# Optimization experiments

Measured on AMD Instinct MI355X. Metric: run time of the kernel, lower is better.

## Reference

```python
import jax, jax.numpy as jnp
import numpy as np
import math

B, S, E, H, D, L, HF = 8, 1024, 512, 8, 64, 6, 2048
EPS = 1e-5
INF = 1000000.0


def _gelu(x):
    # custom tanh-approx gelu from the source
    return 0.5 * x * (1 + jnp.tanh(math.sqrt(2 / math.pi) * (x + 0.044715 * x ** 3)))


def _layernorm(x, gamma, beta):
    mean = jnp.mean(x, axis=-1, keepdims=True)
    var = jnp.mean((x - mean) ** 2, axis=-1, keepdims=True)
    return gamma * ((x - mean) / jnp.sqrt(var + EPS)) + beta


def setup_inputs() -> dict:
    key = jax.random.key(0)
    ks = jax.random.split(key, 10)
    scale = 0.02
    x = jax.random.normal(ks[0], (B, S, E), dtype=jnp.float32)
    att_mask = jax.random.randint(ks[1], (B, S), 0, 2) == 1
    WQ = jax.random.normal(ks[2], (L, E, E), dtype=jnp.float32) * scale
    WK = jax.random.normal(ks[3], (L, E, E), dtype=jnp.float32) * scale
    WV = jax.random.normal(ks[4], (L, E, E), dtype=jnp.float32) * scale
    WO = jax.random.normal(ks[5], (L, E, E), dtype=jnp.float32) * scale
    W1 = jax.random.normal(ks[6], (L, HF, E), dtype=jnp.float32) * scale
    W2 = jax.random.normal(ks[7], (L, E, HF), dtype=jnp.float32) * scale
    bQ = jnp.zeros((L, E)); bK = jnp.zeros((L, E)); bV = jnp.zeros((L, E)); bO = jnp.zeros((L, E))
    b1 = jnp.zeros((L, HF)); b2 = jnp.zeros((L, E))
    g1 = jnp.ones((L, E)); bt1 = jnp.zeros((L, E))
    g2 = jnp.ones((L, E)); bt2 = jnp.zeros((L, E))
    return {"x": x, "att_mask": att_mask, "WQ": WQ, "bQ": bQ, "WK": WK, "bK": bK,
            "WV": WV, "bV": bV, "WO": WO, "bO": bO, "W1": W1, "b1": b1, "W2": W2,
            "b2": b2, "g1": g1, "bt1": bt1, "g2": g2, "bt2": bt2}


def reference(x, att_mask, WQ, bQ, WK, bK, WV, bV, WO, bO, W1, b1, W2, b2, g1, bt1, g2, bt2):
    # additive mask applied to scores: score - (~mask) * infinity, broadcast over (B,1,1,S)
    inv_att = (~att_mask).astype(x.dtype)[:, None, None, :] * INF
    inv_sqrt_d = 1.0 / math.sqrt(D)
    for l in range(L):
        # --- multi-head self-attention ---
        q = (jnp.einsum('bse,fe->bsf', x, WQ[l]) + bQ[l]).reshape(B, S, H, D).transpose(0, 2, 1, 3)
        k = (jnp.einsum('bse,fe->bsf', x, WK[l]) + bK[l]).reshape(B, S, H, D).transpose(0, 2, 1, 3)
        v = (jnp.einsum('bse,fe->bsf', x, WV[l]) + bV[l]).reshape(B, S, H, D).transpose(0, 2, 1, 3)
        score = jnp.einsum('bhsd,bhtd->bhst', q, k) * inv_sqrt_d - inv_att
        attn = jax.nn.softmax(score, axis=-1)
        o = jnp.einsum('bhst,bhtd->bhsd', attn, v).transpose(0, 2, 1, 3).reshape(B, S, E)
        o = jnp.einsum('bse,fe->bsf', o, WO[l]) + bO[l]
        x = _layernorm(x + o, g1[l], bt1[l])
        # --- pointwise feed-forward ---
        h = _gelu(jnp.einsum('bse,fe->bsf', x, W1[l]) + b1[l])
        f = jnp.einsum('bsf,ef->bse', h, W2[l]) + b2[l]
        x = _layernorm(x + f, g2[l], bt2[l])
    return x
```

## Files before the change

kernel.cpp:

```cpp
#include <hip/hip_runtime.h>
#include <cstdint>
#include <cstddef>

#define NB 8
#define NS 1024
#define NE 512
#define NH 8
#define ND 64
#define NL 6
#define NHF 2048
#define NROW (NB*NS)

typedef __bf16 bf16_t;
typedef __bf16 bf8v __attribute__((ext_vector_type(8)));
typedef __bf16 bf4v __attribute__((ext_vector_type(4)));
typedef float  f4   __attribute__((ext_vector_type(4)));

extern "C" __device__ float __ocml_native_exp2_f32(float);
#define EXP2F __ocml_native_exp2_f32
#define LOG2E 1.4426950408889634f

__device__ __forceinline__ void async_copy16(const bf16_t* g, bf16_t* l) {
    __builtin_amdgcn_global_load_lds(
        (const __attribute__((address_space(1))) void*)g,
        (__attribute__((address_space(3))) void*)l,
        16, 0, 0);
}

__device__ __forceinline__ float gelu_f(float x) {
    const float s = fmaf(0.044715f * x * x, x, x);
    const float e = EXP2F(-2.3022081995f * s);
    return x * __builtin_amdgcn_rcpf(1.0f + e);
}

template<int BN, int ACT, int OUT>
__device__ __forceinline__ void gemm_core(
    bf16_t* __restrict__ sm,
    const bf16_t* __restrict__ A, const bf16_t* __restrict__ Bm,
    const float* __restrict__ bias, bf16_t* __restrict__ Cb,
    int m0, int n0, int N, int K)
{
    constexpr int JN = BN / 32, WSPAN = BN / 2;
    bf16_t* As = sm;
    bf16_t* Bs = sm + 2*128*64;
    const int tid  = threadIdx.x;
    const int lane = tid & 63;
    const int wave = tid >> 6;
    const int wm = wave >> 1, wn = wave & 1;
    const int quad = lane >> 4, l16 = lane & 15;
    const int srow = tid >> 3;
    const int scol = (((tid & 7) ^ (srow & 7)) << 3);

    f4 acc[4][JN] = {};

    const bf16_t* Ag = A  + (size_t)(m0 + srow) * K + scol;
    const bf16_t* Bg = Bm + (size_t)(n0 + srow) * K + scol;
    const int sw = (l16 & 7);

    auto stage = [&](int buf, int kt) {
#pragma unroll
        for (int r = 0; r < 4; ++r)
            async_copy16(Ag + (size_t)r * 32 * K + kt, As + buf*8192 + tid*8 + r*2048);
#pragma unroll
        for (int r = 0; r < BN/32; ++r)
            async_copy16(Bg + (size_t)r * 32 * K + kt, Bs + buf*(BN*64) + tid*8 + r*2048);
    };

    stage(0, 0);
    int buf = 0;
    for (int kt = 0; kt < K; kt += 64, buf ^= 1) {
        __syncthreads();
        if (kt + 64 < K) stage(buf ^ 1, kt + 64);
        const bf16_t* Ab = As + buf*8192;
        const bf16_t* Bb = Bs + buf*(BN*64);
#pragma unroll
        for (int s = 0; s < 2; ++s) {
            const int c8 = ((s*4 + quad) ^ sw) * 8;
            bf8v af[4], bfv[JN];
#pragma unroll
            for (int i = 0; i < 4; ++i)
                af[i] = *(const bf8v*)(Ab + (wm*64 + i*16 + l16)*64 + c8);
#pragma unroll
            for (int j = 0; j < JN; ++j)
                bfv[j] = *(const bf8v*)(Bb + (wn*WSPAN + j*16 + l16)*64 + c8);
#pragma unroll
            for (int i = 0; i < 4; ++i)
#pragma unroll
                for (int j = 0; j < JN; ++j)
                    acc[i][j] = __builtin_amdgcn_mfma_f32_16x16x32_bf16(bfv[j], af[i], acc[i][j], 0, 0, 0);
        }
    }

#pragma unroll
    for (int i = 0; i < 4; ++i) {
        const int mi = m0 + wm*64 + i*16 + l16;
        const size_t m = (size_t)mi;
#pragma unroll
        for (int j = 0; j < JN; ++j) {
            const int nb = n0 + wn*WSPAN + j*16 + quad*4;
            const f4 bv = *(const f4*)(bias + nb);
            f4 v = acc[i][j] + bv;
            if (ACT) {
#pragma unroll
                for (int r = 0; r < 4; ++r) v[r] = gelu_f(v[r]);
            }
            bf4v* cp = (bf4v*)(Cb + m * (size_t)N + nb);
            bf4v o;
            if (OUT == 2) {
                const bf4v old = *cp;
#pragma unroll
                for (int r = 0; r < 4; ++r) o[r] = (bf16_t)((float)old[r] + v[r]);
            } else {
#pragma unroll
                for (int r = 0; r < 4; ++r) o[r] = (bf16_t)v[r];
            }
            *cp = o;
        }
    }
}

template<int BN, int ACT, int OUT>
__global__ __launch_bounds__(256)
void gemm_bt_k(const bf16_t* __restrict__ A, const bf16_t* __restrict__ Bm,
               const float* __restrict__ bias, bf16_t* __restrict__ Cb, int N, int K)
{
    __shared__ __align__(16) bf16_t smem[2*128*64 + 2*BN*64];
    gemm_core<BN, ACT, OUT>(smem, A, Bm, bias, Cb,
                            blockIdx.x * 128, blockIdx.y * BN, N, K);
}

__global__ __launch_bounds__(256, 2)
void gemm_qkv_k(const bf16_t* __restrict__ A,
                const bf16_t* __restrict__ wq, const bf16_t* __restrict__ wk, const bf16_t* __restrict__ wv,
                const float* __restrict__ bq, const float* __restrict__ bk, const float* __restrict__ bv,
                bf16_t* __restrict__ Q, bf16_t* __restrict__ K, bf16_t* __restrict__ Vt,
                const unsigned short* __restrict__ rank)
{
    __shared__ __align__(16) bf16_t As_[2*128*64];
    __shared__ __align__(16) bf16_t Bs_[3][2*64*64];
    const int tid  = threadIdx.x;
    const int lane = tid & 63;
    const int wave = tid >> 6;
    const int wm = wave >> 1, wn = wave & 1;
    const int quad = lane >> 4, l16 = lane & 15;
    const int sw = l16 & 7;
    const int srow = tid >> 3;
    const int scol = (((tid & 7) ^ (srow & 7)) << 3);
    const int m0 = blockIdx.x * 128, n0 = blockIdx.y * 64;

    const bf16_t* Ag = A + (size_t)(m0 + srow) * NE + scol;
    const bf16_t* Wg0 = wq + (size_t)(n0 + srow) * NE + scol;
    const bf16_t* Wg1 = wk + (size_t)(n0 + srow) * NE + scol;
    const bf16_t* Wg2 = wv + (size_t)(n0 + srow) * NE + scol;

    f4 acc[3][4][2] = {};

    auto stage = [&](int buf, int kt) {
#pragma unroll
        for (int r = 0; r < 4; ++r)
            async_copy16(Ag + (size_t)r*32*NE + kt, As_ + buf*8192 + tid*8 + r*2048);
#pragma unroll
        for (int r = 0; r < 2; ++r) {
            async_copy16(Wg0 + (size_t)r*32*NE + kt, Bs_[0] + buf*4096 + tid*8 + r*2048);
            async_copy16(Wg1 + (size_t)r*32*NE + kt, Bs_[1] + buf*4096 + tid*8 + r*2048);
            async_copy16(Wg2 + (size_t)r*32*NE + kt, Bs_[2] + buf*4096 + tid*8 + r*2048);
        }
    };

    stage(0, 0);
    int buf = 0;
    for (int kt = 0; kt < NE; kt += 64, buf ^= 1) {
        __syncthreads();
        if (kt + 64 < NE) stage(buf ^ 1, kt + 64);
        const bf16_t* Ab = As_ + buf*8192;
#pragma unroll
        for (int s = 0; s < 2; ++s) {
            const int c8 = ((s*4 + quad) ^ sw) * 8;
            bf8v af[4];
#pragma unroll
            for (int i = 0; i < 4; ++i)
                af[i] = *(const bf8v*)(Ab + (wm*64 + i*16 + l16)*64 + c8);
#pragma unroll
            for (int mat = 0; mat < 3; ++mat) {
                const bf16_t* Bb = Bs_[mat] + buf*4096;
                const bf8v b0 = *(const bf8v*)(Bb + (wn*32      + l16)*64 + c8);
                const bf8v b1 = *(const bf8v*)(Bb + (wn*32 + 16 + l16)*64 + c8);
                if (mat < 2) {
#pragma unroll
                    for (int i = 0; i < 4; ++i) {
                        acc[mat][i][0] = __builtin_amdgcn_mfma_f32_16x16x32_bf16(b0, af[i], acc[mat][i][0], 0, 0, 0);
                        acc[mat][i][1] = __builtin_amdgcn_mfma_f32_16x16x32_bf16(b1, af[i], acc[mat][i][1], 0, 0, 0);
                    }
                } else {
#pragma unroll
                    for (int i = 0; i < 4; ++i) {
                        acc[2][i][0] = __builtin_amdgcn_mfma_f32_16x16x32_bf16(af[i], b0, acc[2][i][0], 0, 0, 0);
                        acc[2][i][1] = __builtin_amdgcn_mfma_f32_16x16x32_bf16(af[i], b1, acc[2][i][1], 0, 0, 0);
                    }
                }
            }
        }
    }

#pragma unroll
    for (int i = 0; i < 4; ++i) {
        const int mi = m0 + wm*64 + i*16 + l16;
        const int mk = (mi & ~1023) + (int)rank[mi];
#pragma unroll
        for (int j = 0; j < 2; ++j) {
            const int nb = n0 + wn*32 + j*16 + quad*4;
            const f4 vq = acc[0][i][j] + *(const f4*)(bq + nb);
            const f4 vk = acc[1][i][j] + *(const f4*)(bk + nb);
            bf4v oq, ok;
#pragma unroll
            for (int r = 0; r < 4; ++r) { oq[r] = (bf16_t)vq[r]; ok[r] = (bf16_t)vk[r]; }
            *(bf4v*)(Q + (size_t)mi * NE + nb) = oq;
            *(bf4v*)(K + (size_t)mk * NE + nb) = ok;
        }
    }
#pragma unroll
    for (int j = 0; j < 2; ++j) {
        const int n = n0 + wn*32 + j*16 + l16;
        const float bvv = bv[n];
#pragma unroll
        for (int i = 0; i < 4; ++i) {
            const int mbase = m0 + wm*64 + i*16 + quad*4;
            const size_t b8h = (size_t)((mbase >> 10)*8 + (n >> 6));
            bf16_t* rowp = Vt + (b8h*64 + (size_t)(n & 63))*1024;
#pragma unroll
            for (int r = 0; r < 4; ++r)
                rowp[rank[mbase + r]] = (bf16_t)(acc[2][i][j][r] + bvv);
        }
    }
}

template<int ACT, int OUT>
__device__ __forceinline__ void gemm256_core(
    bf16_t* __restrict__ sm,
    const bf16_t* __restrict__ A, const bf16_t* __restrict__ Bm,
    const float* __restrict__ bias, bf16_t* __restrict__ Cb,
    int m0, int n0, int N, int K)
{
    const int tid  = threadIdx.x;
    const int lane = tid & 63;
    const int wave = tid >> 6;
    const int wm = wave >> 2, wn = wave & 3;
    const int quad = lane >> 4, l16 = lane & 15;
    const int sw = l16 & 7;
    const int srow = tid >> 3;
    const int scol = ((tid & 7) ^ (srow & 7)) << 3;

    bf16_t* As = sm;
    bf16_t* Bs = sm + 4 * 8192;

    const bf16_t* Ag = A  + (size_t)(m0 + srow) * K + scol;
    const bf16_t* Bg = Bm + (size_t)(n0 + srow) * K + scol;

    auto stageA = [&](int d, int h, int kt) {
        bf16_t* dst = As + (d*2 + h) * 8192 + tid * 8;
        const bf16_t* src = Ag + (size_t)(h * 128) * K + kt;
        async_copy16(src, dst);
        async_copy16(src + (size_t)64 * K, dst + 4096);
    };
    auto stageB = [&](int d, int h, int kt) {
        bf16_t* dst = Bs + (d*2 + h) * 8192 + tid * 8;
        const bf16_t* src = Bg + (size_t)(h * 128) * K + kt;
        async_copy16(src, dst);
        async_copy16(src + (size_t)64 * K, dst + 4096);
    };

    const int nt = K >> 6;

    f4 acc[8][4] = {};
    bf8v bfr[4][2], al[4][2], ah[4][2];

    auto mfmaQ = [&](const bf8v (&af)[4][2], int fb, int gb) {
#pragma unroll
        for (int kh = 0; kh < 2; ++kh)
#pragma unroll
            for (int f = 0; f < 4; ++f)
#pragma unroll
                for (int g = 0; g < 2; ++g)
                    acc[fb+f][gb+g] = __builtin_amdgcn_mfma_f32_16x16x32_bf16(bfr[gb+g][kh], af[f][kh], acc[fb+f][gb+g], 0, 0, 0);
    };

    stageB(0, 0, 0);  stageB(0, 1, 0);  stageA(0, 0, 0);  stageA(0, 1, 0);
    stageB(1, 0, 64); stageB(1, 1, 64); stageA(1, 0, 64);
    asm volatile("s_waitcnt vmcnt(6)" ::: "memory");
    __builtin_amdgcn_s_barrier();

    for (int t = 0; t < nt; ++t) {
        const int d = t & 1;
        const int kt2 = (t + 2) << 6;
        const bf16_t* Ab = As + (d*2 + wm) * 8192;
        const bf16_t* Bb = Bs + (d*2 + (wn >> 1)) * 8192 + (wn & 1) * 4096;

#pragma unroll
        for (int g = 0; g < 4; ++g)
#pragma unroll
            for (int kh = 0; kh < 2; ++kh)
                bfr[g][kh] = *(const bf8v*)(Bb + (g*16 + l16)*64 + (((kh*4 + quad) ^ sw) << 3));
#pragma unroll
        for (int f = 0; f < 4; ++f)
#pragma unroll
            for (int kh = 0; kh < 2; ++kh)
                al[f][kh] = *(const bf8v*)(Ab + (f*16 + l16)*64 + (((kh*4 + quad) ^ sw) << 3));
        if (t + 1 < nt) stageA(d ^ 1, 1, (t + 1) << 6);
        __builtin_amdgcn_s_barrier();
        __builtin_amdgcn_s_setprio(1);
        mfmaQ(al, 0, 0);
        __builtin_amdgcn_s_setprio(0);
        asm volatile("s_waitcnt lgkmcnt(0)" ::: "memory");
        __builtin_amdgcn_s_barrier();

#pragma unroll
        for (int f = 0; f < 4; ++f)
#pragma unroll
            for (int kh = 0; kh < 2; ++kh)
                ah[f][kh] = *(const bf8v*)(Ab + ((f + 4)*16 + l16)*64 + (((kh*4 + quad) ^ sw) << 3));
        if (t + 2 < nt) stageB(d, 0, kt2);
        __builtin_amdgcn_s_barrier();
        __builtin_amdgcn_s_setprio(1);
        mfmaQ(ah, 4, 0);
        __builtin_amdgcn_s_setprio(0);
        asm volatile("s_waitcnt lgkmcnt(0)" ::: "memory");
        __builtin_amdgcn_s_barrier();

        if (t + 2 < nt) stageB(d, 1, kt2);
        __builtin_amdgcn_s_barrier();
        __builtin_amdgcn_s_setprio(1);
        mfmaQ(al, 0, 2);
        __builtin_amdgcn_s_setprio(0);
        asm volatile("s_waitcnt lgkmcnt(0)" ::: "memory");
        __builtin_amdgcn_s_barrier();

        if (t + 2 < nt) stageA(d, 0, kt2);
        __builtin_amdgcn_s_barrier();
        __builtin_amdgcn_s_setprio(1);
        mfmaQ(ah, 4, 2);
        __builtin_amdgcn_s_setprio(0);
        asm volatile("s_waitcnt lgkmcnt(0)" ::: "memory");
        if (t + 1 < nt) {
            if (t + 2 < nt) asm volatile("s_waitcnt vmcnt(6)" ::: "memory");
            else            asm volatile("s_waitcnt vmcnt(0)" ::: "memory");
        }
        __builtin_amdgcn_s_barrier();
    }

#pragma unroll
    for (int f = 0; f < 8; ++f) {
        const int mi = m0 + wm*128 + f*16 + l16;
        const size_t m = (size_t)mi;
#pragma unroll
        for (int g = 0; g < 4; ++g) {
            const int nb = n0 + wn*64 + g*16 + quad*4;
            const f4 bv = *(const f4*)(bias + nb);
            f4 v = acc[f][g] + bv;
            if (ACT) {
#pragma unroll
                for (int r = 0; r < 4; ++r) v[r] = gelu_f(v[r]);
            }
            bf4v* cp = (bf4v*)(Cb + m * (size_t)N + nb);
            bf4v o;
            if (OUT == 2) {
                const bf4v old = *cp;
#pragma unroll
                for (int r = 0; r < 4; ++r) o[r] = (bf16_t)((float)old[r] + v[r]);
            } else {
#pragma unroll
                for (int r = 0; r < 4; ++r) o[r] = (bf16_t)v[r];
            }
            *cp = o;
        }
    }
}

template<int ACT, int OUT>
__global__ __launch_bounds__(512, 2)
void gemm256_k(const bf16_t* __restrict__ A, const bf16_t* __restrict__ Bm,
               const float* __restrict__ bias, bf16_t* __restrict__ Cb, int N, int K)
{
    __shared__ __align__(16) bf16_t smem[8 * 8192];
    gemm256_core<ACT, OUT>(smem, A, Bm, bias, Cb,
                           blockIdx.x * 256, blockIdx.y * 256, N, K);
}

__global__ __launch_bounds__(64)
void pack_k(const int* __restrict__ m, unsigned short* __restrict__ rank,
            int* __restrict__ cntpad, float* __restrict__ maskp)
{
    const int b = blockIdx.x, lane = threadIdx.x;
    unsigned long long bals[16];
    int cnt = 0;
#pragma unroll
    for (int c = 0; c < 16; ++c) {
        const bool mk = m[b*NS + c*64 + lane] != 0;
        bals[c] = __ballot(mk);
        cnt += __popcll(bals[c]);
    }
    int u = 0, kk = 0;
#pragma unroll
    for (int c = 0; c < 16; ++c) {
        const unsigned long long bal = bals[c];
        const bool mk = (bal >> lane) & 1;
        const int pu = __popcll(bal & ((1ull << lane) - 1));
        const int r = mk ? (u + pu) : (cnt + kk + (lane - pu));
        rank[b*NS + c*64 + lane] = (unsigned short)r;
        const int cb = __popcll(bal);
        u += cb; kk += 64 - cb;
    }
    if (lane == 0) {
        int cp = (cnt + 63) & ~63;
        cntpad[b] = cp < 64 ? 64 : cp;
    }
#pragma unroll
    for (int c = 0; c < 16; ++c) {
        const int j = c*64 + lane;
        maskp[b*NS + j] = (j < cnt) ? 0.0f : -1.0e6f * LOG2E;
    }
}

__global__ __launch_bounds__(256)
void attn_k(const bf16_t* __restrict__ Q, const bf16_t* __restrict__ Kg,
            const bf16_t* __restrict__ Vt, const float* __restrict__ maskf,
            const int* __restrict__ cntpad, bf16_t* __restrict__ O)
{
    __shared__ __align__(16) bf16_t Ks[2][64*64];
    __shared__ __align__(16) bf16_t Vs[2][64*64];
    __shared__ __align__(16) bf16_t Ps[4][32*64];
    const int tid  = threadIdx.x;
    const int lane = tid & 63;
    const int wave = tid >> 6;
    const int quad = lane >> 4, l16 = lane & 15;
    const int sw = l16 & 7;
    const int bh = blockIdx.x;
    const int b = bh >> 3, h = bh & 7;
    const int q0 = blockIdx.y * 128;
    const int kend = cntpad[b];

    bf8v qf[2][2];
#pragma unroll
    for (int qi = 0; qi < 2; ++qi) {
        const bf16_t* Qp = Q + (size_t)(b*NS + q0 + wave*32 + qi*16 + l16) * NE + h*ND;
        qf[qi][0] = *(const bf8v*)(Qp + quad*8);
        qf[qi][1] = *(const bf8v*)(Qp + 32 + quad*8);
    }

    f4 oacc[2][4] = {};
    float rs[2] = {0.f, 0.f};

    const int srow = tid >> 3;
    const int scol = (((tid & 7) ^ (srow & 7)) << 3);
    const float c1 = 0.125f * LOG2E;

    auto stage = [&](int buf, int kt) {
#pragma unroll
        for (int r = 0; r < 2; ++r) {
            async_copy16(Kg + (size_t)(b*NS + kt + r*32 + srow) * NE + h*ND + scol,
                         Ks[buf] + (r*256 + tid) * 8);
            async_copy16(Vt + (size_t)(bh*ND + r*32 + srow) * NS + kt + scol,
                         Vs[buf] + (r*256 + tid) * 8);
        }
    };

    stage(0, 0);
    int buf = 0;
    for (int kt = 0; kt < kend; kt += 64, buf ^= 1) {
        __syncthreads();
        if (kt + 64 < kend) stage(buf ^ 1, kt + 64);

        f4 sacc[2][4] = {};
        __builtin_amdgcn_s_setprio(1);
#pragma unroll
        for (int j = 0; j < 4; ++j) {
            bf8v kf0 = *(const bf8v*)(Ks[buf] + (j*16 + l16)*64 + ((quad    ) ^ sw)*8);
            bf8v kf1 = *(const bf8v*)(Ks[buf] + (j*16 + l16)*64 + ((quad + 4) ^ sw)*8);
#pragma unroll
            for (int qi = 0; qi < 2; ++qi) {
                sacc[qi][j] = __builtin_amdgcn_mfma_f32_16x16x32_bf16(kf0, qf[qi][0], sacc[qi][j], 0, 0, 0);
                sacc[qi][j] = __builtin_amdgcn_mfma_f32_16x16x32_bf16(kf1, qf[qi][1], sacc[qi][j], 0, 0, 0);
            }
        }
        __builtin_amdgcn_s_setprio(0);

        bf16_t* Pw = Ps[wave];
#pragma unroll
        for (int j = 0; j < 4; ++j) {
            const f4 mkv = *(const f4*)(maskf + b*NS + kt + j*16 + quad*4);
#pragma unroll
            for (int qi = 0; qi < 2; ++qi) {
                bf4v o;
#pragma unroll
                for (int r = 0; r < 4; ++r) {
                    const float p = EXP2F(fmaf(sacc[qi][j][r], c1, mkv[r]));
                    rs[qi] += p;
                    o[r] = (bf16_t)p;
                }
                const int row = qi*16 + l16;
                const int chunk = (j*2 + (quad >> 1)) ^ sw;
                *(bf4v*)(Pw + row*64 + chunk*8 + (quad & 1)*4) = o;
            }
        }

        __builtin_amdgcn_s_setprio(1);
#pragma unroll
        for (int ks = 0; ks < 2; ++ks) {
            bf8v pf[2];
#pragma unroll
            for (int qi = 0; qi < 2; ++qi)
                pf[qi] = *(const bf8v*)(Pw + (qi*16 + l16)*64 + ((ks*4 + quad) ^ sw)*8);
#pragma unroll
            for (int nt = 0; nt < 4; ++nt) {
                bf8v vf = *(const bf8v*)(Vs[buf] + (nt*16 + l16)*64 + ((ks*4 + quad) ^ sw)*8);
#pragma unroll
                for (int qi = 0; qi < 2; ++qi)
                    oacc[qi][nt] = __builtin_amdgcn_mfma_f32_16x16x32_bf16(vf, pf[qi], oacc[qi][nt], 0, 0, 0);
            }
        }
        __builtin_amdgcn_s_setprio(0);
    }

#pragma unroll
    for (int qi = 0; qi < 2; ++qi) {
        float s = rs[qi];
        s += __shfl_xor(s, 16, 64);
        s += __shfl_xor(s, 32, 64);
        const float inv = 1.0f / s;
        const size_t row = (size_t)(b*NS + q0 + wave*32 + qi*16 + l16);
#pragma unroll
        for (int nt = 0; nt < 4; ++nt) {
            bf4v o;
#pragma unroll
            for (int r = 0; r < 4; ++r) o[r] = (bf16_t)(oacc[qi][nt][r] * inv);
            *(bf4v*)(O + row * NE + h*ND + nt*16 + quad*4) = o;
        }
    }
}

__global__ __launch_bounds__(256)
void ln_k(bf16_t* __restrict__ xb,
          const float* __restrict__ gamma, const float* __restrict__ beta,
          float* __restrict__ fout, int wf)
{
    const int row = blockIdx.x;
    const int tid = threadIdx.x;
    const size_t base = (size_t)row * NE;
    const float x0 = (float)xb[base + tid];
    const float x1 = (float)xb[base + tid + 256];
    float s  = x0 + x1;
    float ss = x0*x0 + x1*x1;
#pragma unroll
    for (int off = 32; off > 0; off >>= 1) {
        s  += __shfl_down(s,  off, 64);
        ss += __shfl_down(ss, off, 64);
    }
    __shared__ float red[8];
    const int wave = tid >> 6;
    if ((tid & 63) == 0) { red[wave] = s; red[4 + wave] = ss; }
    __syncthreads();
    s  = red[0] + red[1] + red[2] + red[3];
    ss = red[4] + red[5] + red[6] + red[7];
    const float mean = s * (1.0f / NE);
    const float var  = ss * (1.0f / NE) - mean * mean;
    const float inv  = rsqrtf(var + 1e-5f);
    const float o0 = gamma[tid]       * ((x0 - mean) * inv) + beta[tid];
    const float o1 = gamma[tid + 256] * ((x1 - mean) * inv) + beta[tid + 256];
    xb[base + tid]       = (bf16_t)o0;
    xb[base + tid + 256] = (bf16_t)o1;
    if (wf) {
        fout[base + tid]       = o0;
        fout[base + tid + 256] = o1;
    }
}

#define W4SZ ((size_t)NL*NE*NE/4)
#define WBSZ ((size_t)NL*NE*NHF/4)
#define XSZ  ((size_t)NROW*NE/4)
#define CVT_TOTAL (4*W4SZ + 2*WBSZ + XSZ)

__global__ void cvt_all(const float* __restrict__ wq, const float* __restrict__ wk,
                        const float* __restrict__ wv, const float* __restrict__ wo,
                        const float* __restrict__ w1, const float* __restrict__ w2,
                        const float* __restrict__ x,
                        bf16_t* __restrict__ owq, bf16_t* __restrict__ owk,
                        bf16_t* __restrict__ owv, bf16_t* __restrict__ owo,
                        bf16_t* __restrict__ ow1, bf16_t* __restrict__ ow2,
                        bf16_t* __restrict__ ox)
{
    size_t i = (size_t)blockIdx.x * 256 + threadIdx.x;
    if (i >= CVT_TOTAL) return;
    const float* src; bf16_t* dst;
    if      (i < 1*W4SZ)           { src = wq; dst = owq; }
    else if (i < 2*W4SZ)           { src = wk; dst = owk; i -= 1*W4SZ; }
    else if (i < 3*W4SZ)           { src = wv; dst = owv; i -= 2*W4SZ; }
    else if (i < 4*W4SZ)           { src = wo; dst = owo; i -= 3*W4SZ; }
    else if (i < 4*W4SZ + WBSZ)    { src = w1; dst = ow1; i -= 4*W4SZ; }
    else if (i < 4*W4SZ + 2*WBSZ)  { src = w2; dst = ow2; i -= 4*W4SZ + WBSZ; }
    else                           { src = x;  dst = ox;  i -= 4*W4SZ + 2*WBSZ; }
    const f4 v = ((const f4*)src)[i];
    bf4v o;
    o[0] = (bf16_t)v[0]; o[1] = (bf16_t)v[1]; o[2] = (bf16_t)v[2]; o[3] = (bf16_t)v[3];
    ((bf4v*)dst)[i] = o;
}

extern "C" void kernel_launch(void* const* d_in, const int* in_sizes, int n_in,
                              void* d_out, int out_size, void* d_ws, size_t ws_size,
                              hipStream_t stream)
{
    (void)in_sizes; (void)n_in; (void)out_size; (void)ws_size;
    const float* x   = (const float*)d_in[0];
    const int*   msk = (const int*)d_in[1];
    const float* WQ = (const float*)d_in[2];  const float* bQ  = (const float*)d_in[3];
    const float* WK = (const float*)d_in[4];  const float* bK  = (const float*)d_in[5];
    const float* WV = (const float*)d_in[6];  const float* bV  = (const float*)d_in[7];
    const float* WO = (const float*)d_in[8];  const float* bO  = (const float*)d_in[9];
    const float* W1 = (const float*)d_in[10]; const float* b1  = (const float*)d_in[11];
    const float* W2 = (const float*)d_in[12]; const float* b2  = (const float*)d_in[13];
    const float* g1 = (const float*)d_in[14]; const float* bt1 = (const float*)d_in[15];
    const float* g2 = (const float*)d_in[16]; const float* bt2 = (const float*)d_in[17];

    char* ws = (char*)d_ws;
    size_t off = 0;
    auto alloc = [&](size_t bytes) { char* p = ws + off; off += (bytes + 255) & ~(size_t)255; return p; };
    bf16_t* xb    = (bf16_t*)alloc((size_t)NROW*NE*2);
    bf16_t* Qb    = (bf16_t*)alloc((size_t)NROW*NE*2);
    bf16_t* Kb    = (bf16_t*)alloc((size_t)NROW*NE*2);
    bf16_t* Vtb   = (bf16_t*)alloc((size_t)NROW*NE*2);
    bf16_t* AOb   = (bf16_t*)alloc((size_t)NROW*NE*2);
    bf16_t* hb    = (bf16_t*)alloc((size_t)NROW*NHF*2);
    bf16_t* wqc   = (bf16_t*)alloc((size_t)NL*NE*NE*2);
    bf16_t* wkc   = (bf16_t*)alloc((size_t)NL*NE*NE*2);
    bf16_t* wvc   = (bf16_t*)alloc((size_t)NL*NE*NE*2);
    bf16_t* woc   = (bf16_t*)alloc((size_t)NL*NE*NE*2);
    bf16_t* w1c   = (bf16_t*)alloc((size_t)NL*NHF*NE*2);
    bf16_t* w2c   = (bf16_t*)alloc((size_t)NL*NE*NHF*2);
    float*  maskp = (float*) alloc((size_t)NB*NS*4);
    unsigned short* rankb = (unsigned short*)alloc((size_t)NB*NS*2);
    int*    cntp  = (int*)   alloc(NB*4);

    cvt_all<<<dim3((unsigned)((CVT_TOTAL + 255) / 256)), dim3(256), 0, stream>>>(
        WQ, WK, WV, WO, W1, W2, x, wqc, wkc, wvc, woc, w1c, w2c, xb);
    pack_k<<<dim3(NB), dim3(64), 0, stream>>>(msk, rankb, cntp, maskp);

    for (int l = 0; l < NL; ++l) {
        const bf16_t* wq  = wqc + (size_t)l*NE*NE;
        const bf16_t* wk  = wkc + (size_t)l*NE*NE;
        const bf16_t* wv  = wvc + (size_t)l*NE*NE;
        const bf16_t* wo  = woc + (size_t)l*NE*NE;
        const bf16_t* w1p = w1c + (size_t)l*NHF*NE;
        const bf16_t* w2p = w2c + (size_t)l*NE*NHF;

        gemm_qkv_k<<<dim3(64, 8), dim3(256), 0, stream>>>(
            xb, wq, wk, wv, bQ + l*NE, bK + l*NE, bV + l*NE, Qb, Kb, Vtb, rankb);
        attn_k<<<dim3(64, 8), dim3(256), 0, stream>>>(Qb, Kb, Vtb, maskp, cntp, AOb);
        gemm_bt_k<128, 0, 2><<<dim3(64, 4), dim3(256), 0, stream>>>(
            AOb, wo, bO + l*NE, xb, NE, NE);
        ln_k<<<dim3(NROW), dim3(256), 0, stream>>>(
            xb, g1 + l*NE, bt1 + l*NE, nullptr, 0);
        gemm256_k<1, 1><<<dim3(32, 8), dim3(512), 0, stream>>>(
            xb, w1p, b1 + l*NHF, hb, NHF, NE);
        gemm_bt_k<128, 0, 2><<<dim3(64, 4), dim3(256), 0, stream>>>(
            hb, w2p, b2 + l*NE, xb, NE, NHF);
        const int last = (l == NL - 1);
        ln_k<<<dim3(NROW), dim3(256), 0, stream>>>(
            xb, g2 + l*NE, bt2 + l*NE, (float*)d_out, last);
    }
}
```

Measured before the change: 933.9 us.

## Fuse output-projection and FFN-down GEMMs with residual add and layernorm

Replaces the generic 128x128 GEMM plus separate layernorm kernels with one kernel. Each block computes a 32-row by full-512-column tile, adds bias and the residual, reduces row statistics across waves through LDS, and writes the normalized bf16 (and optionally fp32) output. This removes two layernorm launches per layer and their extra passes over the activations. In exchange, every block streams the whole weight matrix. The 128KB+ double-buffered LDS footprint limits occupancy, and operand reuse per block drops.

```diff
diff --git a/kernel.cpp b/kernel.cpp
--- a/kernel.cpp
+++ b/kernel.cpp
@@ -33,37 +33,35 @@
     return x * __builtin_amdgcn_rcpf(1.0f + e);
 }
 
-template<int BN, int ACT, int OUT>
-__device__ __forceinline__ void gemm_core(
-    bf16_t* __restrict__ sm,
-    const bf16_t* __restrict__ A, const bf16_t* __restrict__ Bm,
-    const float* __restrict__ bias, bf16_t* __restrict__ Cb,
-    int m0, int n0, int N, int K)
-{
-    constexpr int JN = BN / 32, WSPAN = BN / 2;
-    bf16_t* As = sm;
-    bf16_t* Bs = sm + 2*128*64;
+__global__ __launch_bounds__(512, 2)
+void gemm_rmw_ln_k(const bf16_t* __restrict__ A, const bf16_t* __restrict__ Bm,
+                   const float* __restrict__ bias, bf16_t* __restrict__ xb,
+                   const float* __restrict__ gamma, const float* __restrict__ beta,
+                   float* __restrict__ fout, int wf, int K)
+{
+    __shared__ __align__(16) bf16_t As[2*32*64];
+    __shared__ __align__(16) bf16_t Bs[2*512*64];
+    __shared__ float wsum[8][32], wssq[8][32];
     const int tid  = threadIdx.x;
     const int lane = tid & 63;
     const int wave = tid >> 6;
-    const int wm = wave >> 1, wn = wave & 1;
     const int quad = lane >> 4, l16 = lane & 15;
+    const int sw = l16 & 7;
     const int srow = tid >> 3;
-    const int scol = (((tid & 7) ^ (srow & 7)) << 3);
-
-    f4 acc[4][JN] = {};
+    const int scol = ((tid & 7) ^ (srow & 7)) << 3;
+    const int m0 = blockIdx.x * 32;
 
     const bf16_t* Ag = A  + (size_t)(m0 + srow) * K + scol;
-    const bf16_t* Bg = Bm + (size_t)(n0 + srow) * K + scol;
-    const int sw = (l16 & 7);
+    const bf16_t* Bg = Bm + (size_t)srow * K + scol;
+
+    f4 acc[2][4] = {};
 
     auto stage = [&](int buf, int kt) {
-#pragma unroll
-        for (int r = 0; r < 4; ++r)
-            async_copy16(Ag + (size_t)r * 32 * K + kt, As + buf*8192 + tid*8 + r*2048);
-#pragma unroll
-        for (int r = 0; r < BN/32; ++r)
-            async_copy16(Bg + (size_t)r * 32 * K + kt, Bs + buf*(BN*64) + tid*8 + r*2048);
+        if (tid < 256)
+            async_copy16(Ag + kt, As + buf*2048 + tid*8);
+#pragma unroll
+        for (int r = 0; r < 8; ++r)
+            async_copy16(Bg + (size_t)r * 64 * K + kt, Bs + buf*32768 + (r*512 + tid)*8);
     };
 
     stage(0, 0);
@@ -71,62 +69,85 @@
     for (int kt = 0; kt < K; kt += 64, buf ^= 1) {
         __syncthreads();
         if (kt + 64 < K) stage(buf ^ 1, kt + 64);
-        const bf16_t* Ab = As + buf*8192;
-        const bf16_t* Bb = Bs + buf*(BN*64);
+        const bf16_t* Ab = As + buf*2048;
+        const bf16_t* Bb = Bs + buf*32768;
 #pragma unroll
         for (int s = 0; s < 2; ++s) {
             const int c8 = ((s*4 + quad) ^ sw) * 8;
-            bf8v af[4], bfv[JN];
-#pragma unroll
-            for (int i = 0; i < 4; ++i)
-                af[i] = *(const bf8v*)(Ab + (wm*64 + i*16 + l16)*64 + c8);
-#pragma unroll
-            for (int j = 0; j < JN; ++j)
-                bfv[j] = *(const bf8v*)(Bb + (wn*WSPAN + j*16 + l16)*64 + c8);
-#pragma unroll
-            for (int i = 0; i < 4; ++i)
-#pragma unroll
-                for (int j = 0; j < JN; ++j)
+            bf8v af[2], bfv[4];
+#pragma unroll
+            for (int i = 0; i < 2; ++i)
+                af[i] = *(const bf8v*)(Ab + (i*16 + l16)*64 + c8);
+#pragma unroll
+            for (int j = 0; j < 4; ++j)
+                bfv[j] = *(const bf8v*)(Bb + (wave*64 + j*16 + l16)*64 + c8);
+#pragma unroll
+            for (int i = 0; i < 2; ++i)
+#pragma unroll
+                for (int j = 0; j < 4; ++j)
                     acc[i][j] = __builtin_amdgcn_mfma_f32_16x16x32_bf16(bfv[j], af[i], acc[i][j], 0, 0, 0);
         }
     }
 
-#pragma unroll
-    for (int i = 0; i < 4; ++i) {
-        const int mi = m0 + wm*64 + i*16 + l16;
-        const size_t m = (size_t)mi;
-#pragma unroll
-        for (int j = 0; j < JN; ++j) {
-            const int nb = n0 + wn*WSPAN + j*16 + quad*4;
+    f4 v[2][4];
+    float ps[2], pss[2];
+#pragma unroll
+    for (int i = 0; i < 2; ++i) {
+        ps[i] = 0.f; pss[i] = 0.f;
+        const size_t m = (size_t)(m0 + i*16 + l16);
+#pragma unroll
+        for (int j = 0; j < 4; ++j) {
+            const int nb = wave*64 + j*16 + quad*4;
             const f4 bv = *(const f4*)(bias + nb);
-            f4 v = acc[i][j] + bv;
-            if (ACT) {
-#pragma unroll
-                for (int r = 0; r < 4; ++r) v[r] = gelu_f(v[r]);
-            }
-            bf4v* cp = (bf4v*)(Cb + m * (size_t)N + nb);
-            bf4v o;
-            if (OUT == 2) {
-                const bf4v old = *cp;
-#pragma unroll
-                for (int r = 0; r < 4; ++r) o[r] = (bf16_t)((float)old[r] + v[r]);
-            } else {
-#pragma unroll
-                for (int r = 0; r < 4; ++r) o[r] = (bf16_t)v[r];
-            }
-            *cp = o;
-        }
-    }
-}
-
-template<int BN, int ACT, int OUT>
-__global__ __launch_bounds__(256)
-void gemm_bt_k(const bf16_t* __restrict__ A, const bf16_t* __restrict__ Bm,
-               const float* __restrict__ bias, bf16_t* __restrict__ Cb, int N, int K)
-{
-    __shared__ __align__(16) bf16_t smem[2*128*64 + 2*BN*64];
-    gemm_core<BN, ACT, OUT>(smem, A, Bm, bias, Cb,
-                            blockIdx.x * 128, blockIdx.y * BN, N, K);
+            const bf4v old = *(const bf4v*)(xb + m * NE + nb);
+            f4 t = acc[i][j] + bv;
+#pragma unroll
+            for (int r = 0; r < 4; ++r) {
+                t[r] += (float)old[r];
+                ps[i]  += t[r];
+                pss[i] += t[r] * t[r];
+            }
+            v[i][j] = t;
+        }
+        ps[i]  += __shfl_xor(ps[i], 16, 64);
+        ps[i]  += __shfl_xor(ps[i], 32, 64);
+        pss[i] += __shfl_xor(pss[i], 16, 64);
+        pss[i] += __shfl_xor(pss[i], 32, 64);
+    }
+    if (quad == 0) {
+#pragma unroll
+        for (int i = 0; i < 2; ++i) {
+            wsum[wave][i*16 + l16] = ps[i];
+            wssq[wave][i*16 + l16] = pss[i];
+        }
+    }
+    __syncthreads();
+#pragma unroll
+    for (int i = 0; i < 2; ++i) {
+        const int row = i*16 + l16;
+        float s = 0.f, ss = 0.f;
+#pragma unroll
+        for (int w = 0; w < 8; ++w) { s += wsum[w][row]; ss += wssq[w][row]; }
+        const float mean = s * (1.0f / NE);
+        const float var  = ss * (1.0f / NE) - mean * mean;
+        const float inv  = rsqrtf(var + 1e-5f);
+        const size_t m = (size_t)(m0 + row);
+#pragma unroll
+        for (int j = 0; j < 4; ++j) {
+            const int nb = wave*64 + j*16 + quad*4;
+            const f4 gm = *(const f4*)(gamma + nb);
+            const f4 bt = *(const f4*)(beta + nb);
+            f4 o;
+            bf4v ob;
+#pragma unroll
+            for (int r = 0; r < 4; ++r) {
+                o[r]  = gm[r] * ((v[i][j][r] - mean) * inv) + bt[r];
+                ob[r] = (bf16_t)o[r];
+            }
+            *(bf4v*)(xb + m * NE + nb) = ob;
+            if (wf) *(f4*)(fout + m * NE + nb) = o;
+        }
+    }
 }
 
 __global__ __launch_bounds__(256, 2)
@@ -534,42 +555,6 @@
             for (int r = 0; r < 4; ++r) o[r] = (bf16_t)(oacc[qi][nt][r] * inv);
             *(bf4v*)(O + row * NE + h*ND + nt*16 + quad*4) = o;
         }
-    }
-}
-
-__global__ __launch_bounds__(256)
-void ln_k(bf16_t* __restrict__ xb,
-          const float* __restrict__ gamma, const float* __restrict__ beta,
-          float* __restrict__ fout, int wf)
-{
-    const int row = blockIdx.x;
-    const int tid = threadIdx.x;
-    const size_t base = (size_t)row * NE;
-    const float x0 = (float)xb[base + tid];
-    const float x1 = (float)xb[base + tid + 256];
-    float s  = x0 + x1;
-    float ss = x0*x0 + x1*x1;
-#pragma unroll
-    for (int off = 32; off > 0; off >>= 1) {
-        s  += __shfl_down(s,  off, 64);
-        ss += __shfl_down(ss, off, 64);
-    }
-    __shared__ float red[8];
-    const int wave = tid >> 6;
-    if ((tid & 63) == 0) { red[wave] = s; red[4 + wave] = ss; }
-    __syncthreads();
-    s  = red[0] + red[1] + red[2] + red[3];
-    ss = red[4] + red[5] + red[6] + red[7];
-    const float mean = s * (1.0f / NE);
-    const float var  = ss * (1.0f / NE) - mean * mean;
-    const float inv  = rsqrtf(var + 1e-5f);
-    const float o0 = gamma[tid]       * ((x0 - mean) * inv) + beta[tid];
-    const float o1 = gamma[tid + 256] * ((x1 - mean) * inv) + beta[tid + 256];
-    xb[base + tid]       = (bf16_t)o0;
-    xb[base + tid + 256] = (bf16_t)o1;
-    if (wf) {
-        fout[base + tid]       = o0;
-        fout[base + tid + 256] = o1;
     }
 }
 
@@ -649,20 +634,18 @@
         const bf16_t* wo  = woc + (size_t)l*NE*NE;
         const bf16_t* w1p = w1c + (size_t)l*NHF*NE;
         const bf16_t* w2p = w2c + (size_t)l*NE*NHF;
+        const int last = (l == NL - 1);
 
         gemm_qkv_k<<<dim3(64, 8), dim3(256), 0, stream>>>(
             xb, wq, wk, wv, bQ + l*NE, bK + l*NE, bV + l*NE, Qb, Kb, Vtb, rankb);
         attn_k<<<dim3(64, 8), dim3(256), 0, stream>>>(Qb, Kb, Vtb, maskp, cntp, AOb);
-        gemm_bt_k<128, 0, 2><<<dim3(64, 4), dim3(256), 0, stream>>>(
-            AOb, wo, bO + l*NE, xb, NE, NE);
-        ln_k<<<dim3(NROW), dim3(256), 0, stream>>>(
-            xb, g1 + l*NE, bt1 + l*NE, nullptr, 0);
+        gemm_rmw_ln_k<<<dim3(256), dim3(512), 0, stream>>>(
+            AOb, wo, bO + l*NE, xb, g1 + l*NE, bt1 + l*NE,
+            nullptr, 0, NE);
         gemm256_k<1, 1><<<dim3(32, 8), dim3(512), 0, stream>>>(
             xb, w1p, b1 + l*NHF, hb, NHF, NE);
-        gemm_bt_k<128, 0, 2><<<dim3(64, 4), dim3(256), 0, stream>>>(
-            hb, w2p, b2 + l*NE, xb, NE, NHF);
-        const int last = (l == NL - 1);
-        ln_k<<<dim3(NROW), dim3(256), 0, stream>>>(
-            xb, g2 + l*NE, bt2 + l*NE, (float*)d_out, last);
-    }
-}
+        gemm_rmw_ln_k<<<dim3(256), dim3(512), 0, stream>>>(
+            hb, w2p, b2 + l*NE, xb, g2 + l*NE, bt2 + l*NE,
+            (float*)d_out, last, NHF);
+    }
+}
```

Result: slower. 975.7 us (+4.5%).

## Fuse output projection with residual add and first layernorm

Applied to the files above, without the earlier changes.

Adds a GEMM kernel that computes a full 512-wide output row tile (32 rows per block), adds bias and the residual, and applies layernorm in the epilogue using cross-wave reductions through shared memory. This replaces the separate WO GEMM plus ln_k launch after attention, so the intermediate bf16 round trip and one kernel launch per layer go away. In exchange the grid shrinks to 256 blocks with a large B tile (64KB of LDS per stage), which may lower occupancy and parallelism. Variance is now computed as E[x^2]-mean^2 in one pass.

```diff
diff --git a/kernel.cpp b/kernel.cpp
--- a/kernel.cpp
+++ b/kernel.cpp
@@ -127,6 +127,123 @@
     __shared__ __align__(16) bf16_t smem[2*128*64 + 2*BN*64];
     gemm_core<BN, ACT, OUT>(smem, A, Bm, bias, Cb,
                             blockIdx.x * 128, blockIdx.y * BN, N, K);
+}
+
+__global__ __launch_bounds__(512, 2)
+void gemm_rmw_ln_k(const bf16_t* __restrict__ A, const bf16_t* __restrict__ Bm,
+                   const float* __restrict__ bias, bf16_t* __restrict__ xb,
+                   const float* __restrict__ gamma, const float* __restrict__ beta,
+                   float* __restrict__ fout, int wf, int K)
+{
+    __shared__ __align__(16) bf16_t As[2*32*64];
+    __shared__ __align__(16) bf16_t Bs[2*512*64];
+    __shared__ float wsum[8][32], wssq[8][32];
+    const int tid  = threadIdx.x;
+    const int lane = tid & 63;
+    const int wave = tid >> 6;
+    const int quad = lane >> 4, l16 = lane & 15;
+    const int sw = l16 & 7;
+    const int srow = tid >> 3;
+    const int scol = ((tid & 7) ^ (srow & 7)) << 3;
+    const int m0 = blockIdx.x * 32;
+
+    const bf16_t* Ag = A  + (size_t)(m0 + srow) * K + scol;
+    const bf16_t* Bg = Bm + (size_t)srow * K + scol;
+
+    f4 acc[2][4] = {};
+
+    auto stage = [&](int buf, int kt) {
+        if (tid < 256)
+            async_copy16(Ag + kt, As + buf*2048 + tid*8);
+#pragma unroll
+        for (int r = 0; r < 8; ++r)
+            async_copy16(Bg + (size_t)r * 64 * K + kt, Bs + buf*32768 + (r*512 + tid)*8);
+    };
+
+    stage(0, 0);
+    int buf = 0;
+    for (int kt = 0; kt < K; kt += 64, buf ^= 1) {
+        __syncthreads();
+        if (kt + 64 < K) stage(buf ^ 1, kt + 64);
+        const bf16_t* Ab = As + buf*2048;
+        const bf16_t* Bb = Bs + buf*32768;
+#pragma unroll
+        for (int s = 0; s < 2; ++s) {
+            const int c8 = ((s*4 + quad) ^ sw) * 8;
+            bf8v af[2], bfv[4];
+#pragma unroll
+            for (int i = 0; i < 2; ++i)
+                af[i] = *(const bf8v*)(Ab + (i*16 + l16)*64 + c8);
+#pragma unroll
+            for (int j = 0; j < 4; ++j)
+                bfv[j] = *(const bf8v*)(Bb + (wave*64 + j*16 + l16)*64 + c8);
+#pragma unroll
+            for (int i = 0; i < 2; ++i)
+#pragma unroll
+                for (int j = 0; j < 4; ++j)
+                    acc[i][j] = __builtin_amdgcn_mfma_f32_16x16x32_bf16(bfv[j], af[i], acc[i][j], 0, 0, 0);
+        }
+    }
+
+    f4 v[2][4];
+    float ps[2], pss[2];
+#pragma unroll
+    for (int i = 0; i < 2; ++i) {
+        ps[i] = 0.f; pss[i] = 0.f;
+        const size_t m = (size_t)(m0 + i*16 + l16);
+#pragma unroll
+        for (int j = 0; j < 4; ++j) {
+            const int nb = wave*64 + j*16 + quad*4;
+            const f4 bv = *(const f4*)(bias + nb);
+            const bf4v old = *(const bf4v*)(xb + m * NE + nb);
+            f4 t = acc[i][j] + bv;
+#pragma unroll
+            for (int r = 0; r < 4; ++r) {
+                t[r] += (float)old[r];
+                ps[i]  += t[r];
+                pss[i] += t[r] * t[r];
+            }
+            v[i][j] = t;
+        }
+        ps[i]  += __shfl_xor(ps[i], 16, 64);
+        ps[i]  += __shfl_xor(ps[i], 32, 64);
+        pss[i] += __shfl_xor(pss[i], 16, 64);
+        pss[i] += __shfl_xor(pss[i], 32, 64);
+    }
+    if (quad == 0) {
+#pragma unroll
+        for (int i = 0; i < 2; ++i) {
+            wsum[wave][i*16 + l16] = ps[i];
+            wssq[wave][i*16 + l16] = pss[i];
+        }
+    }
+    __syncthreads();
+#pragma unroll
+    for (int i = 0; i < 2; ++i) {
+        const int row = i*16 + l16;
+        float s = 0.f, ss = 0.f;
+#pragma unroll
+        for (int w = 0; w < 8; ++w) { s += wsum[w][row]; ss += wssq[w][row]; }
+        const float mean = s * (1.0f / NE);
+        const float var  = ss * (1.0f / NE) - mean * mean;
+        const float inv  = rsqrtf(var + 1e-5f);
+        const size_t m = (size_t)(m0 + row);
+#pragma unroll
+        for (int j = 0; j < 4; ++j) {
+            const int nb = wave*64 + j*16 + quad*4;
+            const f4 gm = *(const f4*)(gamma + nb);
+            const f4 bt = *(const f4*)(beta + nb);
+            f4 o;
+            bf4v ob;
+#pragma unroll
+            for (int r = 0; r < 4; ++r) {
+                o[r]  = gm[r] * ((v[i][j][r] - mean) * inv) + bt[r];
+                ob[r] = (bf16_t)o[r];
+            }
+            *(bf4v*)(xb + m * NE + nb) = ob;
+            if (wf) *(f4*)(fout + m * NE + nb) = o;
+        }
+    }
 }
 
 __global__ __launch_bounds__(256, 2)
@@ -649,19 +766,18 @@
         const bf16_t* wo  = woc + (size_t)l*NE*NE;
         const bf16_t* w1p = w1c + (size_t)l*NHF*NE;
         const bf16_t* w2p = w2c + (size_t)l*NE*NHF;
+        const int last = (l == NL - 1);
 
         gemm_qkv_k<<<dim3(64, 8), dim3(256), 0, stream>>>(
             xb, wq, wk, wv, bQ + l*NE, bK + l*NE, bV + l*NE, Qb, Kb, Vtb, rankb);
         attn_k<<<dim3(64, 8), dim3(256), 0, stream>>>(Qb, Kb, Vtb, maskp, cntp, AOb);
-        gemm_bt_k<128, 0, 2><<<dim3(64, 4), dim3(256), 0, stream>>>(
-            AOb, wo, bO + l*NE, xb, NE, NE);
-        ln_k<<<dim3(NROW), dim3(256), 0, stream>>>(
-            xb, g1 + l*NE, bt1 + l*NE, nullptr, 0);
+        gemm_rmw_ln_k<<<dim3(256), dim3(512), 0, stream>>>(
+            AOb, wo, bO + l*NE, xb, g1 + l*NE, bt1 + l*NE,
+            nullptr, 0, NE);
         gemm256_k<1, 1><<<dim3(32, 8), dim3(512), 0, stream>>>(
             xb, w1p, b1 + l*NHF, hb, NHF, NE);
         gemm_bt_k<128, 0, 2><<<dim3(64, 4), dim3(256), 0, stream>>>(
             hb, w2p, b2 + l*NE, xb, NE, NHF);
-        const int last = (l == NL - 1);
         ln_k<<<dim3(NROW), dim3(256), 0, stream>>>(
             xb, g2 + l*NE, bt2 + l*NE, (float*)d_out, last);
     }
```

Result: no change. 916.3 us (-1.9%).
